# Performance work log

Hardware: AMD Instinct MI355X
Metric: run time of the kernel (lower is better)

Reference implementation:

```python
import jax, jax.numpy as jnp
import numpy as np

B, S, CL, DIM, HEADS, FFN = 2, 2048, 512, 2048, 16, 8192
EPS = 1e-6


def rms_norm(x, w):
    return x * jax.lax.rsqrt(jnp.mean(x * x, axis=-1, keepdims=True) + EPS) * w


def mha(q, k, v, num_heads):
    b, sq, d = q.shape
    sk = k.shape[1]
    hd = d // num_heads
    q = q.reshape(b, sq, num_heads, hd)
    k = k.reshape(b, sk, num_heads, hd)
    v = v.reshape(b, sk, num_heads, hd)
    attn = jnp.einsum('bqhd,bkhd->bhqk', q, k) * (hd ** -0.5)
    attn = jax.nn.softmax(attn, axis=-1)
    out = jnp.einsum('bhqk,bkhd->bqhd', attn, v)
    return out.reshape(b, sq, d)


def setup_inputs() -> dict:
    key = jax.random.key(0)
    ks = iter(jax.random.split(key, 48))
    nrm = lambda shape, scale: jax.random.normal(next(ks), shape, jnp.float32) * scale
    w_scale = DIM ** -0.5
    inp = {
        'x': nrm((B, S, DIM), 1.0),
        'e': nrm((B, 6, DIM), 0.5),
        'context': nrm((B, CL, DIM), 1.0),
        'modulation': nrm((1, 6, DIM), w_scale),
        'norm1_w': jnp.ones((DIM,), jnp.float32),
        'norm2_w': jnp.ones((DIM,), jnp.float32),
        'norm3_w': jnp.ones((DIM,), jnp.float32),
        'sa_nq_w': jnp.ones((DIM,), jnp.float32),
        'sa_nk_w': jnp.ones((DIM,), jnp.float32),
        'ffn_norm_w': jnp.ones((DIM,), jnp.float32),
        'sa_qw': nrm((DIM, DIM), w_scale), 'sa_qb': jnp.zeros((DIM,), jnp.float32),
        'sa_kw': nrm((DIM, DIM), w_scale), 'sa_kb': jnp.zeros((DIM,), jnp.float32),
        'sa_vw': nrm((DIM, DIM), w_scale), 'sa_vb': jnp.zeros((DIM,), jnp.float32),
        'sa_ow': nrm((DIM, DIM), w_scale), 'sa_ob': jnp.zeros((DIM,), jnp.float32),
        'ca_qw': nrm((DIM, DIM), w_scale), 'ca_qb': jnp.zeros((DIM,), jnp.float32),
        'ca_kw': nrm((DIM, DIM), w_scale), 'ca_kb': jnp.zeros((DIM,), jnp.float32),
        'ca_vw': nrm((DIM, DIM), w_scale), 'ca_vb': jnp.zeros((DIM,), jnp.float32),
        'ca_ow': nrm((DIM, DIM), w_scale), 'ca_ob': jnp.zeros((DIM,), jnp.float32),
        'ffn_w1': nrm((DIM, FFN), w_scale), 'ffn_b1': jnp.zeros((FFN,), jnp.float32),
        'ffn_w2': nrm((FFN, DIM), FFN ** -0.5), 'ffn_b2': jnp.zeros((DIM,), jnp.float32),
    }
    return inp


def reference(x, e, context, modulation, norm1_w, norm2_w, norm3_w, sa_nq_w, sa_nk_w,
              ffn_norm_w, sa_qw, sa_qb, sa_kw, sa_kb, sa_vw, sa_vb, sa_ow, sa_ob,
              ca_qw, ca_qb, ca_kw, ca_kb, ca_vw, ca_vb, ca_ow, ca_ob,
              ffn_w1, ffn_b1, ffn_w2, ffn_b2):
    # AdaLN modulation: (modulation + e) chunked into 6 along dim=1 -> each [B,1,DIM]
    mod = modulation + e
    e0, e1, e2, e3, e4, e5 = [mod[:, i:i + 1, :] for i in range(6)]

    # --- self attention with qk_norm=True ---
    h = rms_norm(x, norm1_w) * (1.0 + e1) + e0
    q = rms_norm(h @ sa_qw + sa_qb, sa_nq_w)
    k = rms_norm(h @ sa_kw + sa_kb, sa_nk_w)
    v = h @ sa_vw + sa_vb
    y = mha(q, k, v, HEADS) @ sa_ow + sa_ob
    x = x + y * e2

    # --- cross attention (cross_attn_norm=False, no qk norm) ---
    h = rms_norm(x, norm2_w)
    q = h @ ca_qw + ca_qb
    k = context @ ca_kw + ca_kb
    v = context @ ca_vw + ca_vb
    y = mha(q, k, v, HEADS) @ ca_ow + ca_ob
    x = x + y

    # --- FFN: modulate(norm3(x)) -> RMSNorm -> Linear -> GELU(tanh) -> Linear ---
    h = rms_norm(x, norm3_w) * (1.0 + e4) + e3
    h = rms_norm(h, ffn_norm_w)
    h = jax.nn.gelu(h @ ffn_w1 + ffn_b1, approximate=True)
    y = h @ ffn_w2 + ffn_b2
    x = x + y * e5
    return x
```

## Files before the change

kernel.cpp:

```cpp
#include <hip/hip_runtime.h>
#include <hip/hip_bf16.h>
#include <cstdint>

#define DIM   2048
#define HEADS 16
#define HD    128
#define SEQ   2048
#define CLEN  512
#define FFND  8192
#define BATCH 2

using bf16 = __hip_bfloat16;
typedef __attribute__((ext_vector_type(8))) short  short8;
typedef __attribute__((ext_vector_type(4))) short  short4v;
typedef __attribute__((ext_vector_type(4))) float  f32x4;
typedef __attribute__((ext_vector_type(8))) __bf16 bf16x8;

__device__ __forceinline__ short f2bs(float f){ bf16 h = __float2bfloat16(f); return __builtin_bit_cast(short, h); }
__device__ __forceinline__ float bs2f(short s){ return __builtin_bit_cast(float, (uint32_t)((uint16_t)s) << 16); }

__device__ __forceinline__ f32x4 mfma16(short8 a, short8 b, f32x4 c){
  return __builtin_amdgcn_mfma_f32_16x16x32_bf16(
      __builtin_bit_cast(bf16x8, a), __builtin_bit_cast(bf16x8, b), c, 0, 0, 0);
}

__device__ __forceinline__ void gload_lds16(const void* g, const void* l){
  __builtin_amdgcn_global_load_lds(
      (const __attribute__((address_space(1))) void*)(uintptr_t)g,
      (__attribute__((address_space(3))) void*)(uint32_t)(uintptr_t)l, 16, 0, 0);
}

__device__ __forceinline__ float block_sum(float v, float* sbuf, int tid){
  #pragma unroll
  for (int m = 32; m >= 1; m >>= 1) v += __shfl_xor(v, m, 64);
  const int w = tid >> 6;
  if ((tid & 63) == 0) sbuf[w] = v;
  __syncthreads();
  float r = sbuf[0] + sbuf[1] + sbuf[2] + sbuf[3];
  __syncthreads();
  return r;
}


__global__ void modadd_k(const float* __restrict__ m, const float* __restrict__ e,
                         float* __restrict__ out){
  int i = blockIdx.x * 256 + threadIdx.x;
  out[i] = m[i % (6 * DIM)] + e[i];
}

__global__ void f2b8_k(const float* __restrict__ in, bf16* __restrict__ out){
  int i = blockIdx.x * 256 + threadIdx.x;
  const float4* p = (const float4*)in;
  float4 a = p[2*i], c = p[2*i+1];
  short8 o;
  o[0]=f2bs(a.x); o[1]=f2bs(a.y); o[2]=f2bs(a.z); o[3]=f2bs(a.w);
  o[4]=f2bs(c.x); o[5]=f2bs(c.y); o[6]=f2bs(c.z); o[7]=f2bs(c.w);
  *((short8*)out + i) = o;
}

__global__ void biascat_k(const float* __restrict__ b0, const float* __restrict__ b1,
                          const float* __restrict__ b2, const float* __restrict__ c0,
                          const float* __restrict__ c1, float* __restrict__ bcat,
                          float* __restrict__ bcat2){
  int i = blockIdx.x * 256 + threadIdx.x;
  if (i < 3*DIM){
    const float* src = (i < DIM) ? b0 : (i < 2*DIM) ? b1 : b2;
    bcat[i] = src[i & (DIM-1)];
  } else {
    int j = i - 3*DIM;
    const float* src = (j < DIM) ? c0 : c1;
    bcat2[j] = src[j & (DIM-1)];
  }
}

__global__ __launch_bounds__(256) void transpose_w(const float* __restrict__ W,
                                                   bf16* __restrict__ Wt, int K, int N){
  __shared__ float tile[32][33];
  const int tx = threadIdx.x & 31, ty = threadIdx.x >> 5;
  const size_t k0 = blockIdx.y * 32, n0 = blockIdx.x * 32;
  #pragma unroll
  for (int i = 0; i < 4; i++)
    tile[ty + i*8][tx] = W[(k0 + ty + i*8) * (size_t)N + n0 + tx];
  __syncthreads();
  #pragma unroll
  for (int i = 0; i < 4; i++)
    Wt[(n0 + ty + i*8) * (size_t)K + k0 + tx] = __float2bfloat16(tile[tx][ty + i*8]);
}

__global__ __launch_bounds__(256) void transpose_w3(const float* __restrict__ W0,
    const float* __restrict__ W1, const float* __restrict__ W2,
    bf16* __restrict__ Wt, int K, int N){
  __shared__ float tile[32][33];
  const float* W = (blockIdx.z == 0) ? W0 : (blockIdx.z == 1) ? W1 : W2;
  bf16* dst = Wt + (size_t)blockIdx.z * K * N;
  const int tx = threadIdx.x & 31, ty = threadIdx.x >> 5;
  const size_t k0 = blockIdx.y * 32, n0 = blockIdx.x * 32;
  #pragma unroll
  for (int i = 0; i < 4; i++)
    tile[ty + i*8][tx] = W[(k0 + ty + i*8) * (size_t)N + n0 + tx];
  __syncthreads();
  #pragma unroll
  for (int i = 0; i < 4; i++)
    dst[(n0 + ty + i*8) * (size_t)K + k0 + tx] = __float2bfloat16(tile[tx][ty + i*8]);
}

template<int MODE>
__global__ __launch_bounds__(256) void norm_x(const float* __restrict__ x,
    const float* __restrict__ w1, const float* __restrict__ w2,
    const float* __restrict__ mod, bf16* __restrict__ out, int S)
{
  const int row = blockIdx.x, tid = threadIdx.x;
  const int b = row / S;
  __shared__ float sbuf[4];
  const float* xr = x + (size_t)row * DIM;
  float v[8];
  #pragma unroll
  for (int i = 0; i < 2; i++){
    float4 t = *(const float4*)(xr + i*1024 + tid*4);
    v[i*4+0]=t.x; v[i*4+1]=t.y; v[i*4+2]=t.z; v[i*4+3]=t.w;
  }
  float ss = 0.f;
  #pragma unroll
  for (int j = 0; j < 8; j++) ss += v[j]*v[j];
  ss = block_sum(ss, sbuf, tid);
  const float r = rsqrtf(ss * (1.0f/DIM) + 1e-6f);
  const float* mb = mod + (size_t)b * 6 * DIM;
  float t8[8];
  #pragma unroll
  for (int i = 0; i < 2; i++)
    #pragma unroll
    for (int j = 0; j < 4; j++){
      int n = i*1024 + tid*4 + j;
      float val = v[i*4+j] * r * w1[n];
      if (MODE == 1) val = val * (1.f + mb[DIM + n]) + mb[n];
      if (MODE == 3) val = val * (1.f + mb[4*DIM + n]) + mb[3*DIM + n];
      t8[i*4+j] = val;
    }
  if (MODE == 3){
    float s2 = 0.f;
    #pragma unroll
    for (int j = 0; j < 8; j++) s2 += t8[j]*t8[j];
    s2 = block_sum(s2, sbuf, tid);
    const float r2 = rsqrtf(s2 * (1.0f/DIM) + 1e-6f);
    #pragma unroll
    for (int i = 0; i < 2; i++)
      #pragma unroll
      for (int j = 0; j < 4; j++){
        int n = i*1024 + tid*4 + j;
        t8[i*4+j] = t8[i*4+j] * r2 * w2[n];
      }
  }
  #pragma unroll
  for (int i = 0; i < 2; i++){
    short4v o;
    #pragma unroll
    for (int j = 0; j < 4; j++) o[j] = f2bs(t8[i*4+j]);
    *(short4v*)(out + (size_t)row*DIM + i*1024 + tid*4) = o;
  }
}

__global__ __launch_bounds__(256) void rmsnorm2_bf16_ip(bf16* __restrict__ xq, const float* __restrict__ wq,
                                                        bf16* __restrict__ xk, const float* __restrict__ wk,
                                                        int M){
  const int row = blockIdx.x, tid = threadIdx.x;
  __shared__ float sbuf[4];
  bf16* xr; const float* w;
  if (row < M){ xr = xq + (size_t)row * DIM; w = wq; }
  else        { xr = xk + (size_t)(row - M) * DIM; w = wk; }
  short8 v = *(const short8*)(xr + tid*8);
  float f[8]; float ss = 0.f;
  #pragma unroll
  for (int j = 0; j < 8; j++){ f[j] = bs2f(v[j]); ss += f[j]*f[j]; }
  ss = block_sum(ss, sbuf, tid);
  const float r = rsqrtf(ss * (1.0f/DIM) + 1e-6f);
  short8 o;
  #pragma unroll
  for (int j = 0; j < 8; j++) o[j] = f2bs(f[j] * r * w[tid*8 + j]);
  *(short8*)(xr + tid*8) = o;
}

#define GBUF 24576
template<int EPI>
__global__ __launch_bounds__(512, 2) void gemm_bf16(
    const bf16* __restrict__ A, const bf16* __restrict__ Bt,
    const float* __restrict__ bias, const float* __restrict__ xin,
    const float* __restrict__ mod, float* __restrict__ outf,
    bf16* __restrict__ outb, bf16* __restrict__ out1, bf16* __restrict__ out2,
    int M, int N, int K, int S_tok, int eidx)
{
  __shared__ __align__(16) char lds[3][GBUF];
  const int tid = threadIdx.x;
  const int w = tid >> 6, l = tid & 63;
  const int lrow = l & 15, lhi = l >> 4;
  const int wm = w >> 2, wn = w & 3;
  const size_t m0 = (size_t)blockIdx.y * 128, n0 = (size_t)blockIdx.x * 256;

  f32x4 acc[4][4] = {};

  auto gofs = [&](int sid){ return (size_t)(sid >> 2) * K + (size_t)(((sid & 3) ^ ((sid >> 3) & 3)) * 8); };
  const bf16* gA0 = A  + m0 * K + gofs(tid);
  const bf16* gB0 = Bt + n0 * K + gofs(tid);
  const bf16* gB1 = Bt + n0 * K + gofs(tid + 512);

  auto stage = [&](int kt, char* buf){
    const size_t ko = (size_t)kt * 32;
    gload_lds16(gA0 + ko, buf + tid * 16);
    gload_lds16(gB0 + ko, buf + 8192 + tid * 16);
    gload_lds16(gB1 + ko, buf + 8192 + (tid + 512) * 16);
  };

  const int nt = K >> 5;
  stage(0, lds[0]);
  stage(1, lds[1]);
  asm volatile("s_waitcnt vmcnt(3)" ::: "memory");
  __builtin_amdgcn_s_barrier();
  __builtin_amdgcn_sched_barrier(0);

  const int sread = (lhi ^ ((lrow >> 1) & 3)) * 16;

  int bi = 0;
  for (int t = 0; t < nt; ++t){
    const char* br = lds[bi];
    const bool st = (t + 2 < nt);
    if (st){
      int wi = bi + 2; if (wi >= 3) wi -= 3;
      stage(t + 2, lds[wi]);
    }
    short8 af[4], bf[4];
    #pragma unroll
    for (int mi = 0; mi < 4; mi++)
      af[mi] = *(const short8*)(br + (wm*64 + mi*16 + lrow)*64 + sread);
    #pragma unroll
    for (int ni = 0; ni < 4; ni++)
      bf[ni] = *(const short8*)(br + 8192 + (wn*64 + ni*16 + lrow)*64 + sread);
    __builtin_amdgcn_s_setprio(1);
    #pragma unroll
    for (int mi = 0; mi < 4; mi++)
      #pragma unroll
      for (int ni = 0; ni < 4; ni++)
        acc[mi][ni] = mfma16(af[mi], bf[ni], acc[mi][ni]);
    __builtin_amdgcn_s_setprio(0);
    if (st)               { asm volatile("s_waitcnt vmcnt(3)" ::: "memory"); }
    else if (t + 1 < nt)  { asm volatile("s_waitcnt vmcnt(0)" ::: "memory"); }
    __builtin_amdgcn_s_barrier();
    __builtin_amdgcn_sched_barrier(0);
    bi = (bi + 1 == 3) ? 0 : bi + 1;
  }

  #pragma unroll
  for (int mi = 0; mi < 4; mi++)
    #pragma unroll
    for (int ni = 0; ni < 4; ni++)
      #pragma unroll
      for (int r = 0; r < 4; r++){
        const size_t m = m0 + wm*64 + mi*16 + lhi*4 + r;
        const size_t n = n0 + wn*64 + ni*16 + lrow;
        float v = acc[mi][ni][r] + bias[n];
        if constexpr (EPI == 0) {
          outb[m * N + n] = __float2bfloat16(v);
        } else if constexpr (EPI == 1) {
          const size_t b = m / S_tok, s = m % S_tok;
          const size_t h = n >> 7, d = n & 127;
          outb[((b*HEADS + h)*HD + d) * S_tok + s] = __float2bfloat16(v);
        } else if constexpr (EPI == 2) {
          const float ev = mod[(m / S_tok) * 6 * DIM + (size_t)eidx * DIM + n];
          outf[m * N + n] = xin[m * N + n] + v * ev;
        } else if constexpr (EPI == 3) {
          outf[m * N + n] += v;
        } else if constexpr (EPI == 4) {
          float u = 0.7978845608028654f * (v + 0.044715f * v * v * v);
          outb[m * N + n] = __float2bfloat16(0.5f * v * (1.0f + tanhf(u)));
        } else if constexpr (EPI == 5) {
          const size_t sg = n >> 11, col = n & 2047;
          if (sg == 0)      outb[m * DIM + col] = __float2bfloat16(v);
          else if (sg == 1) out1[m * DIM + col] = __float2bfloat16(v);
          else {
            const size_t b = m / S_tok, s = m % S_tok;
            const size_t h = col >> 7, d = col & 127;
            out2[((b*HEADS + h)*HD + d) * S_tok + s] = __float2bfloat16(v);
          }
        } else {
          const size_t sg = n >> 11, col = n & 2047;
          if (sg == 0) out1[m * DIM + col] = __float2bfloat16(v);
          else {
            const size_t b = m / S_tok, s = m % S_tok;
            const size_t h = col >> 7, d = col & 127;
            out2[((b*HEADS + h)*HD + d) * S_tok + s] = __float2bfloat16(v);
          }
        }
      }
}

__global__ __launch_bounds__(256, 2) void attn_fwd(
    const bf16* __restrict__ Q, const bf16* __restrict__ Kp, const bf16* __restrict__ Vt,
    bf16* __restrict__ O, int SQ, int SKV)
{
  const int tid = threadIdx.x, w = tid >> 6, l = tid & 63;
  const int lrow = l & 15, lhi = l >> 4;
  const int nwg = gridDim.x;
  const int p = blockIdx.x;
  const int f = (p & 7) * (nwg >> 3) + (p >> 3);
  const int nqb = SQ >> 7;
  const int xq = f % nqb;
  const int h  = (f / nqb) % HEADS;
  const int b  = f / (nqb * HEADS);
  const int q0 = xq * 128 + w * 32;

  __shared__ __align__(16) char kls[2][16384];
  __shared__ __align__(16) char vls[16384];
  __shared__ __align__(16) bf16 P[4][2][16][72];
  const float scale = 0.08838834764831845f;

  short8 qf[2][4];
  #pragma unroll
  for (int g = 0; g < 2; g++){
    const bf16* qp = Q + ((size_t)(b*SQ + q0 + g*16 + lrow))*DIM + h*HD + lhi*8;
    #pragma unroll
    for (int ds = 0; ds < 4; ds++) qf[g][ds] = *(const short8*)(qp + ds*32);
  }

  const bf16* kg = Kp + (size_t)b*SKV*DIM + h*HD;
  const bf16* vg = Vt + (size_t)(b*HEADS + h)*HD*SKV;

  f32x4 acc[2][8] = {};
  float m_run[2] = {-INFINITY, -INFINITY}, l_run[2] = {0.f, 0.f};
  const int nt = SKV >> 6;

  auto stage_k = [&](int buf, int kv0){
    char* kd = &kls[buf][0];
    #pragma unroll
    for (int i = 0; i < 4; i++){
      int sid = i*256 + tid;
      int row = sid >> 4, sg = sid & 15;
      int gsg = sg ^ (row & 7);
      gload_lds16(kg + (size_t)(kv0 + row)*DIM + gsg*8, kd + sid*16);
    }
  };
  auto stage_v = [&](int kv0){
    #pragma unroll
    for (int i = 0; i < 4; i++){
      int sid = i*256 + tid;
      int d = sid >> 3, sg = sid & 7;
      int gsg = sg ^ (d & 7);
      gload_lds16(vg + (size_t)d*SKV + kv0 + gsg*8, &vls[0] + sid*16);
    }
  };

  stage_k(0, 0);
  stage_v(0);
  asm volatile("s_waitcnt vmcnt(0)" ::: "memory");
  __builtin_amdgcn_s_barrier();

  for (int t = 0; t < nt; ++t){
    if (t > 0)      stage_v(t * 64);
    if (t + 1 < nt) stage_k((t + 1) & 1, (t + 1) * 64);
    const char* kb = &kls[t & 1][0];

    f32x4 st[2][4] = {};
    #pragma unroll
    for (int kvf = 0; kvf < 4; kvf++){
      const int row = kvf*16 + lrow;
      const int rx = row & 7;
      #pragma unroll
      for (int ds = 0; ds < 4; ds++){
        const int seg = (ds*4 + lhi) ^ rx;
        short8 kf = *(const short8*)(kb + row*256 + seg*16);
        st[0][kvf] = mfma16(kf, qf[0][ds], st[0][kvf]);
        st[1][kvf] = mfma16(kf, qf[1][ds], st[1][kvf]);
      }
    }

    #pragma unroll
    for (int g = 0; g < 2; g++){
      float sv[16]; float smax = -INFINITY;
      #pragma unroll
      for (int kvf = 0; kvf < 4; kvf++)
        #pragma unroll
        for (int r = 0; r < 4; r++){
          float xv = st[g][kvf][r] * scale;
          sv[kvf*4+r] = xv; smax = fmaxf(smax, xv);
        }
      smax = fmaxf(smax, __shfl_xor(smax, 16, 64));
      smax = fmaxf(smax, __shfl_xor(smax, 32, 64));
      const float mnew = fmaxf(m_run[g], smax);
      const float corr = __expf(m_run[g] - mnew);
      float psum = 0.f;
      #pragma unroll
      for (int i = 0; i < 16; i++){ float pe = __expf(sv[i] - mnew); sv[i] = pe; psum += pe; }
      psum += __shfl_xor(psum, 16, 64); psum += __shfl_xor(psum, 32, 64);
      l_run[g] = l_run[g] * corr + psum;
      m_run[g] = mnew;
      #pragma unroll
      for (int kvf = 0; kvf < 4; kvf++){
        short4v o;
        #pragma unroll
        for (int r = 0; r < 4; r++) o[r] = f2bs(sv[kvf*4+r]);
        *(short4v*)&P[w][g][lrow][kvf*16 + lhi*4] = o;
      }
      float cr[4];
      #pragma unroll
      for (int r = 0; r < 4; r++) cr[r] = __shfl(corr, lhi*4 + r, 64);
      #pragma unroll
      for (int df = 0; df < 8; df++){
        acc[g][df][0] *= cr[0]; acc[g][df][1] *= cr[1];
        acc[g][df][2] *= cr[2]; acc[g][df][3] *= cr[3];
      }
    }

    if (t + 1 < nt) { asm volatile("s_waitcnt vmcnt(4)" ::: "memory"); }
    else            { asm volatile("s_waitcnt vmcnt(0)" ::: "memory"); }
    __builtin_amdgcn_s_barrier();
    asm volatile("s_waitcnt lgkmcnt(0)" ::: "memory");
    __builtin_amdgcn_sched_barrier(0);

    short8 pf[2][2];
    #pragma unroll
    for (int g = 0; g < 2; g++){
      pf[g][0] = *(const short8*)&P[w][g][lrow][lhi*8];
      pf[g][1] = *(const short8*)&P[w][g][lrow][32 + lhi*8];
    }
    #pragma unroll
    for (int df = 0; df < 8; df++){
      const int d = df*16 + lrow;
      const int dx = d & 7;
      short8 vf0 = *(const short8*)(&vls[0] + d*128 + ((lhi)     ^ dx)*16);
      short8 vf1 = *(const short8*)(&vls[0] + d*128 + ((lhi + 4) ^ dx)*16);
      acc[0][df] = mfma16(pf[0][0], vf0, acc[0][df]);
      acc[0][df] = mfma16(pf[0][1], vf1, acc[0][df]);
      acc[1][df] = mfma16(pf[1][0], vf0, acc[1][df]);
      acc[1][df] = mfma16(pf[1][1], vf1, acc[1][df]);
    }
    if (t + 1 < nt) { asm volatile("s_waitcnt vmcnt(0)" ::: "memory"); }
    __builtin_amdgcn_s_barrier();
  }

  #pragma unroll
  for (int g = 0; g < 2; g++){
    const float linv = 1.0f / l_run[g];
    float li[4];
    #pragma unroll
    for (int r = 0; r < 4; r++) li[r] = __shfl(linv, lhi*4 + r, 64);
    #pragma unroll
    for (int df = 0; df < 8; df++)
      #pragma unroll
      for (int r = 0; r < 4; r++){
        const size_t q = q0 + g*16 + lhi*4 + r;
        O[((size_t)(b*SQ + q))*DIM + h*HD + df*16 + lrow] = __float2bfloat16(acc[g][df][r] * li[r]);
      }
  }
}


extern "C" void kernel_launch(void* const* d_in, const int* in_sizes, int n_in,
                              void* d_out, int out_size, void* d_ws, size_t ws_size,
                              hipStream_t stream)
{
  const float* x    = (const float*)d_in[0];
  const float* e    = (const float*)d_in[1];
  const float* ctx  = (const float*)d_in[2];
  const float* modw = (const float*)d_in[3];
  const float* n1w  = (const float*)d_in[4];
  const float* n2w  = (const float*)d_in[5];
  const float* n3w  = (const float*)d_in[6];
  const float* nqw  = (const float*)d_in[7];
  const float* nkw  = (const float*)d_in[8];
  const float* fnw  = (const float*)d_in[9];
  const float* saqw = (const float*)d_in[10]; const float* saqb = (const float*)d_in[11];
  const float* sakw = (const float*)d_in[12]; const float* sakb = (const float*)d_in[13];
  const float* savw = (const float*)d_in[14]; const float* savb = (const float*)d_in[15];
  const float* saow = (const float*)d_in[16]; const float* saob = (const float*)d_in[17];
  const float* caqw = (const float*)d_in[18]; const float* caqb = (const float*)d_in[19];
  const float* cakw = (const float*)d_in[20]; const float* cakb = (const float*)d_in[21];
  const float* cavw = (const float*)d_in[22]; const float* cavb = (const float*)d_in[23];
  const float* caow = (const float*)d_in[24]; const float* caob = (const float*)d_in[25];
  const float* fw1  = (const float*)d_in[26]; const float* fb1  = (const float*)d_in[27];
  const float* fw2  = (const float*)d_in[28]; const float* fb2  = (const float*)d_in[29];
  float* out = (float*)d_out;
  (void)in_sizes; (void)n_in; (void)out_size; (void)ws_size;

  char* ws = (char*)d_ws;
  size_t off = 0;
  auto alloc = [&](size_t bytes) -> void* {
    void* p = ws + off; off = (off + bytes + 255) & ~(size_t)255; return p;
  };
  bf16*  wt   = (bf16*)alloc((size_t)FFND * DIM * 2);
  float* mod  = (float*)alloc((size_t)BATCH * 6 * DIM * 4);
  float* bcat = (float*)alloc((size_t)3 * DIM * 4);
  float* bcat2= (float*)alloc((size_t)2 * DIM * 4);
  bf16*  ctxb = (bf16*)alloc((size_t)BATCH * CLEN * DIM * 2);
  bf16*  hbuf = (bf16*)alloc((size_t)BATCH * SEQ * DIM * 2);
  bf16*  qbuf = (bf16*)alloc((size_t)BATCH * SEQ * DIM * 2);
  bf16*  kbuf = (bf16*)alloc((size_t)BATCH * SEQ * DIM * 2);
  bf16*  vtb  = (bf16*)alloc((size_t)BATCH * SEQ * DIM * 2);
  bf16*  aout = (bf16*)alloc((size_t)BATCH * SEQ * DIM * 2);
  float* xcur = (float*)alloc((size_t)BATCH * SEQ * DIM * 4);
  bf16*  hf   = (bf16*)alloc((size_t)BATCH * SEQ * FFND * 2);

  const int M = BATCH * SEQ;
  const int Mc = BATCH * CLEN;

  modadd_k<<<dim3(96), dim3(256), 0, stream>>>(modw, e, mod);
  f2b8_k<<<dim3(1024), dim3(256), 0, stream>>>(ctx, ctxb);
  biascat_k<<<dim3(40), dim3(256), 0, stream>>>(saqb, sakb, savb, cakb, cavb, bcat, bcat2);

  norm_x<1><<<dim3(M), dim3(256), 0, stream>>>(x, n1w, nullptr, mod, hbuf, SEQ);

  transpose_w3<<<dim3(DIM/32, DIM/32, 3), dim3(256), 0, stream>>>(saqw, sakw, savw, wt, DIM, DIM);
  gemm_bf16<5><<<dim3(3*DIM/256, M/128), dim3(512), 0, stream>>>(hbuf, wt, bcat, nullptr, nullptr, nullptr, qbuf, kbuf, vtb, M, 3*DIM, DIM, SEQ, 0);
  rmsnorm2_bf16_ip<<<dim3(2*M), dim3(256), 0, stream>>>(qbuf, nqw, kbuf, nkw, M);

  attn_fwd<<<dim3((SEQ/128)*HEADS*BATCH), dim3(256), 0, stream>>>(qbuf, kbuf, vtb, aout, SEQ, SEQ);

  transpose_w<<<dim3(DIM/32, DIM/32), dim3(256), 0, stream>>>(saow, wt, DIM, DIM);
  gemm_bf16<2><<<dim3(DIM/256, M/128), dim3(512), 0, stream>>>(aout, wt, saob, x, mod, xcur, nullptr, nullptr, nullptr, M, DIM, DIM, SEQ, 2);

  norm_x<2><<<dim3(M), dim3(256), 0, stream>>>(xcur, n2w, nullptr, mod, hbuf, SEQ);

  transpose_w3<<<dim3(DIM/32, DIM/32, 3), dim3(256), 0, stream>>>(caqw, cakw, cavw, wt, DIM, DIM);
  gemm_bf16<0><<<dim3(DIM/256, M/128), dim3(512), 0, stream>>>(hbuf, wt, caqb, nullptr, nullptr, nullptr, qbuf, nullptr, nullptr, M, DIM, DIM, SEQ, 0);
  gemm_bf16<6><<<dim3(2*DIM/256, Mc/128), dim3(512), 0, stream>>>(ctxb, wt + (size_t)DIM*DIM, bcat2, nullptr, nullptr, nullptr, nullptr, kbuf, vtb, Mc, 2*DIM, DIM, CLEN, 0);

  attn_fwd<<<dim3((SEQ/128)*HEADS*BATCH), dim3(256), 0, stream>>>(qbuf, kbuf, vtb, aout, SEQ, CLEN);

  transpose_w<<<dim3(DIM/32, DIM/32), dim3(256), 0, stream>>>(caow, wt, DIM, DIM);
  gemm_bf16<3><<<dim3(DIM/256, M/128), dim3(512), 0, stream>>>(aout, wt, caob, nullptr, nullptr, xcur, nullptr, nullptr, nullptr, M, DIM, DIM, SEQ, 0);

  norm_x<3><<<dim3(M), dim3(256), 0, stream>>>(xcur, n3w, fnw, mod, hbuf, SEQ);

  transpose_w<<<dim3(FFND/32, DIM/32), dim3(256), 0, stream>>>(fw1, wt, DIM, FFND);
  gemm_bf16<4><<<dim3(FFND/256, M/128), dim3(512), 0, stream>>>(hbuf, wt, fb1, nullptr, nullptr, nullptr, hf, nullptr, nullptr, M, FFND, DIM, SEQ, 0);

  transpose_w<<<dim3(DIM/32, FFND/32), dim3(256), 0, stream>>>(fw2, wt, FFND, DIM);
  gemm_bf16<2><<<dim3(DIM/256, M/128), dim3(512), 0, stream>>>(hf, wt, fb2, xcur, mod, out, nullptr, nullptr, nullptr, M, DIM, FFND, SEQ, 5);
}
```

Before: 897.6 us.

## Widen weight transpose tiles, lazily rescale softmax, prioritize MFMA waves in attention

The weight transpose kernels move to 64x64 tiles and write four bf16 values per store instead of scalar stores, which cuts launch count and narrow global writes. The flash-attention loop skips the running-max update and accumulator rescale when every lane's new max stays within 8 of the current one, so the exp correction and shuffles are avoided on most tiles. It also raises wave priority around the MFMA blocks with s_setprio. The lazy rescale lets the exponentials grow to about e^8 before renormalising, which relies on fp32 and bf16 range for the P values.

After: 886.3 us, median of 2. About the same (-1.3%).

```diff
diff --git a/kernel.cpp b/kernel.cpp
--- a/kernel.cpp
+++ b/kernel.cpp
@@ -75,33 +75,47 @@
 
 __global__ __launch_bounds__(256) void transpose_w(const float* __restrict__ W,
                                                    bf16* __restrict__ Wt, int K, int N){
-  __shared__ float tile[32][33];
-  const int tx = threadIdx.x & 31, ty = threadIdx.x >> 5;
-  const size_t k0 = blockIdx.y * 32, n0 = blockIdx.x * 32;
-  #pragma unroll
-  for (int i = 0; i < 4; i++)
-    tile[ty + i*8][tx] = W[(k0 + ty + i*8) * (size_t)N + n0 + tx];
+  __shared__ float tile[64][65];
+  const int tx = threadIdx.x & 63, ty = threadIdx.x >> 6;
+  const size_t k0 = (size_t)blockIdx.y * 64, n0 = (size_t)blockIdx.x * 64;
+  #pragma unroll
+  for (int i = 0; i < 16; i++)
+    tile[ty + i*4][tx] = W[(k0 + ty + i*4) * (size_t)N + n0 + tx];
   __syncthreads();
-  #pragma unroll
-  for (int i = 0; i < 4; i++)
-    Wt[(n0 + ty + i*8) * (size_t)K + k0 + tx] = __float2bfloat16(tile[tx][ty + i*8]);
+  const int kx = threadIdx.x & 15;
+  const int ny = threadIdx.x >> 4;
+  #pragma unroll
+  for (int i = 0; i < 4; i++){
+    const int n = ny + i*16;
+    short4v o;
+    #pragma unroll
+    for (int j = 0; j < 4; j++) o[j] = f2bs(tile[kx*4 + j][n]);
+    *(short4v*)&Wt[(n0 + n) * (size_t)K + k0 + kx*4] = o;
+  }
 }
 
 __global__ __launch_bounds__(256) void transpose_w3(const float* __restrict__ W0,
     const float* __restrict__ W1, const float* __restrict__ W2,
     bf16* __restrict__ Wt, int K, int N){
-  __shared__ float tile[32][33];
+  __shared__ float tile[64][65];
   const float* W = (blockIdx.z == 0) ? W0 : (blockIdx.z == 1) ? W1 : W2;
   bf16* dst = Wt + (size_t)blockIdx.z * K * N;
-  const int tx = threadIdx.x & 31, ty = threadIdx.x >> 5;
-  const size_t k0 = blockIdx.y * 32, n0 = blockIdx.x * 32;
-  #pragma unroll
-  for (int i = 0; i < 4; i++)
-    tile[ty + i*8][tx] = W[(k0 + ty + i*8) * (size_t)N + n0 + tx];
+  const int tx = threadIdx.x & 63, ty = threadIdx.x >> 6;
+  const size_t k0 = (size_t)blockIdx.y * 64, n0 = (size_t)blockIdx.x * 64;
+  #pragma unroll
+  for (int i = 0; i < 16; i++)
+    tile[ty + i*4][tx] = W[(k0 + ty + i*4) * (size_t)N + n0 + tx];
   __syncthreads();
-  #pragma unroll
-  for (int i = 0; i < 4; i++)
-    dst[(n0 + ty + i*8) * (size_t)K + k0 + tx] = __float2bfloat16(tile[tx][ty + i*8]);
+  const int kx = threadIdx.x & 15;
+  const int ny = threadIdx.x >> 4;
+  #pragma unroll
+  for (int i = 0; i < 4; i++){
+    const int n = ny + i*16;
+    short4v o;
+    #pragma unroll
+    for (int j = 0; j < 4; j++) o[j] = f2bs(tile[kx*4 + j][n]);
+    *(short4v*)&dst[(n0 + n) * (size_t)K + k0 + kx*4] = o;
+  }
 }
 
 template<int MODE>
@@ -357,6 +371,7 @@
     const char* kb = &kls[t & 1][0];
 
     f32x4 st[2][4] = {};
+    __builtin_amdgcn_s_setprio(1);
     #pragma unroll
     for (int kvf = 0; kvf < 4; kvf++){
       const int row = kvf*16 + lrow;
@@ -369,6 +384,7 @@
         st[1][kvf] = mfma16(kf, qf[1][ds], st[1][kvf]);
       }
     }
+    __builtin_amdgcn_s_setprio(0);
 
     #pragma unroll
     for (int g = 0; g < 2; g++){
@@ -382,14 +398,12 @@
         }
       smax = fmaxf(smax, __shfl_xor(smax, 16, 64));
       smax = fmaxf(smax, __shfl_xor(smax, 32, 64));
-      const float mnew = fmaxf(m_run[g], smax);
-      const float corr = __expf(m_run[g] - mnew);
+      const bool nore = __all(smax <= m_run[g] + 8.0f);
+      const float mnew = nore ? m_run[g] : fmaxf(m_run[g], smax);
       float psum = 0.f;
       #pragma unroll
       for (int i = 0; i < 16; i++){ float pe = __expf(sv[i] - mnew); sv[i] = pe; psum += pe; }
       psum += __shfl_xor(psum, 16, 64); psum += __shfl_xor(psum, 32, 64);
-      l_run[g] = l_run[g] * corr + psum;
-      m_run[g] = mnew;
       #pragma unroll
       for (int kvf = 0; kvf < 4; kvf++){
         short4v o;
@@ -397,13 +411,20 @@
         for (int r = 0; r < 4; r++) o[r] = f2bs(sv[kvf*4+r]);
         *(short4v*)&P[w][g][lrow][kvf*16 + lhi*4] = o;
       }
-      float cr[4];
-      #pragma unroll
-      for (int r = 0; r < 4; r++) cr[r] = __shfl(corr, lhi*4 + r, 64);
-      #pragma unroll
-      for (int df = 0; df < 8; df++){
-        acc[g][df][0] *= cr[0]; acc[g][df][1] *= cr[1];
-        acc[g][df][2] *= cr[2]; acc[g][df][3] *= cr[3];
+      if (nore){
+        l_run[g] += psum;
+      } else {
+        const float corr = __expf(m_run[g] - mnew);
+        l_run[g] = l_run[g] * corr + psum;
+        m_run[g] = mnew;
+        float cr[4];
+        #pragma unroll
+        for (int r = 0; r < 4; r++) cr[r] = __shfl(corr, lhi*4 + r, 64);
+        #pragma unroll
+        for (int df = 0; df < 8; df++){
+          acc[g][df][0] *= cr[0]; acc[g][df][1] *= cr[1];
+          acc[g][df][2] *= cr[2]; acc[g][df][3] *= cr[3];
+        }
       }
     }
 
@@ -419,6 +440,7 @@
       pf[g][0] = *(const short8*)&P[w][g][lrow][lhi*8];
       pf[g][1] = *(const short8*)&P[w][g][lrow][32 + lhi*8];
     }
+    __builtin_amdgcn_s_setprio(1);
     #pragma unroll
     for (int df = 0; df < 8; df++){
       const int d = df*16 + lrow;
@@ -430,6 +452,7 @@
       acc[1][df] = mfma16(pf[1][0], vf0, acc[1][df]);
       acc[1][df] = mfma16(pf[1][1], vf1, acc[1][df]);
     }
+    __builtin_amdgcn_s_setprio(0);
     if (t + 1 < nt) { asm volatile("s_waitcnt vmcnt(0)" ::: "memory"); }
     __builtin_amdgcn_s_barrier();
   }
@@ -505,31 +528,31 @@
 
   norm_x<1><<<dim3(M), dim3(256), 0, stream>>>(x, n1w, nullptr, mod, hbuf, SEQ);
 
-  transpose_w3<<<dim3(DIM/32, DIM/32, 3), dim3(256), 0, stream>>>(saqw, sakw, savw, wt, DIM, DIM);
+  transpose_w3<<<dim3(DIM/64, DIM/64, 3), dim3(256), 0, stream>>>(saqw, sakw, savw, wt, DIM, DIM);
   gemm_bf16<5><<<dim3(3*DIM/256, M/128), dim3(512), 0, stream>>>(hbuf, wt, bcat, nullptr, nullptr, nullptr, qbuf, kbuf, vtb, M, 3*DIM, DIM, SEQ, 0);
   rmsnorm2_bf16_ip<<<dim3(2*M), dim3(256), 0, stream>>>(qbuf, nqw, kbuf, nkw, M);
 
   attn_fwd<<<dim3((SEQ/128)*HEADS*BATCH), dim3(256), 0, stream>>>(qbuf, kbuf, vtb, aout, SEQ, SEQ);
 
-  transpose_w<<<dim3(DIM/32, DIM/32), dim3(256), 0, stream>>>(saow, wt, DIM, DIM);
+  transpose_w<<<dim3(DIM/64, DIM/64), dim3(256), 0, stream>>>(saow, wt, DIM, DIM);
   gemm_bf16<2><<<dim3(DIM/256, M/128), dim3(512), 0, stream>>>(aout, wt, saob, x, mod, xcur, nullptr, nullptr, nullptr, M, DIM, DIM, SEQ, 2);
 
   norm_x<2><<<dim3(M), dim3(256), 0, stream>>>(xcur, n2w, nullptr, mod, hbuf, SEQ);
 
-  transpose_w3<<<dim3(DIM/32, DIM/32, 3), dim3(256), 0, stream>>>(caqw, cakw, cavw, wt, DIM, DIM);
+  transpose_w3<<<dim3(DIM/64, DIM/64, 3), dim3(256), 0, stream>>>(caqw, cakw, cavw, wt, DIM, DIM);
   gemm_bf16<0><<<dim3(DIM/256, M/128), dim3(512), 0, stream>>>(hbuf, wt, caqb, nullptr, nullptr, nullptr, qbuf, nullptr, nullptr, M, DIM, DIM, SEQ, 0);
   gemm_bf16<6><<<dim3(2*DIM/256, Mc/128), dim3(512), 0, stream>>>(ctxb, wt + (size_t)DIM*DIM, bcat2, nullptr, nullptr, nullptr, nullptr, kbuf, vtb, Mc, 2*DIM, DIM, CLEN, 0);
 
   attn_fwd<<<dim3((SEQ/128)*HEADS*BATCH), dim3(256), 0, stream>>>(qbuf, kbuf, vtb, aout, SEQ, CLEN);
 
-  transpose_w<<<dim3(DIM/32, DIM/32), dim3(256), 0, stream>>>(caow, wt, DIM, DIM);
+  transpose_w<<<dim3(DIM/64, DIM/64), dim3(256), 0, stream>>>(caow, wt, DIM, DIM);
   gemm_bf16<3><<<dim3(DIM/256, M/128), dim3(512), 0, stream>>>(aout, wt, caob, nullptr, nullptr, xcur, nullptr, nullptr, nullptr, M, DIM, DIM, SEQ, 0);
 
   norm_x<3><<<dim3(M), dim3(256), 0, stream>>>(xcur, n3w, fnw, mod, hbuf, SEQ);
 
-  transpose_w<<<dim3(FFND/32, DIM/32), dim3(256), 0, stream>>>(fw1, wt, DIM, FFND);
+  transpose_w<<<dim3(FFND/64, DIM/64), dim3(256), 0, stream>>>(fw1, wt, DIM, FFND);
   gemm_bf16<4><<<dim3(FFND/256, M/128), dim3(512), 0, stream>>>(hbuf, wt, fb1, nullptr, nullptr, nullptr, hf, nullptr, nullptr, M, FFND, DIM, SEQ, 0);
 
-  transpose_w<<<dim3(DIM/32, FFND/32), dim3(256), 0, stream>>>(fw2, wt, FFND, DIM);
+  transpose_w<<<dim3(DIM/64, FFND/64), dim3(256), 0, stream>>>(fw2, wt, FFND, DIM);
   gemm_bf16<2><<<dim3(DIM/256, M/128), dim3(512), 0, stream>>>(hf, wt, fb2, xcur, mod, out, nullptr, nullptr, nullptr, M, DIM, FFND, SEQ, 5);
 }
```
